# Performance work log

Hardware: AMD Instinct MI355X
Metric: run time of the kernel (lower is better)

## Reference

```python
import jax, jax.numpy as jnp
import numpy as np
from jax import lax

B, T, E = 2, 2048, 2048
H, D = 16, 128
C = H * D          # qk_dim == v_dim == 2048
K = 4              # short conv kernel size
EPS = 1e-5


def setup_inputs() -> dict:
    key = jax.random.key(0)
    ks = jax.random.split(key, 11)
    s = 0.02
    return {
        "x": jax.random.normal(ks[0], (B, T, E), dtype=jnp.float32),
        "recurrent_state": jnp.zeros((B, H, D, D), dtype=jnp.float32),
        "Wq": jax.random.normal(ks[1], (C, E), dtype=jnp.float32) * s,
        "Wk": jax.random.normal(ks[2], (C, E), dtype=jnp.float32) * s,
        "Wv": jax.random.normal(ks[3], (C, E), dtype=jnp.float32) * s,
        "Wbeta": jax.random.normal(ks[4], (H, E), dtype=jnp.float32) * s,
        "Wgate": jax.random.normal(ks[5], (C, E), dtype=jnp.float32) * s,
        "Wo": jax.random.normal(ks[6], (E, C), dtype=jnp.float32) * s,
        "wq_conv": jax.random.normal(ks[7], (C, 1, K), dtype=jnp.float32) * 0.5,
        "wk_conv": jax.random.normal(ks[8], (C, 1, K), dtype=jnp.float32) * 0.5,
        "wv_conv": jax.random.normal(ks[9], (C, 1, K), dtype=jnp.float32) * 0.5,
    }


def _causal_dwconv(u, w):
    # u: (B, T, C), w: (C, 1, K). Torch pads both sides by K-1 then truncates
    # to length T -> equivalent to causal left-pad of K-1.
    u = u.transpose(0, 2, 1)  # (B, C, T)
    y = lax.conv_general_dilated(
        u, w, window_strides=(1,), padding=[(K - 1, 0)],
        feature_group_count=C, dimension_numbers=("NCH", "OIH", "NCH"))
    return y.transpose(0, 2, 1)  # (B, T, C)


def _delta_scan(q, k, v, beta, state):
    # q,k,v: (B,T,H,D); beta: (B,T,H); state: (B,H,D,D)
    def step(S, inp):
        qt, kt, vt, bt = inp  # (B,H,D),(B,H,D),(B,H,D),(B,H)
        b = bt[..., None, None]
        S = (1.0 - b) * S + b * (kt[..., :, None] * vt[..., None, :])  # bhde
        o = jnp.einsum("bhde,bhd->bhe", S, qt)
        return S, o

    xs = (q.transpose(1, 0, 2, 3), k.transpose(1, 0, 2, 3),
          v.transpose(1, 0, 2, 3), beta.transpose(1, 0, 2))
    final_state, outs = lax.scan(step, state, xs)
    return outs.transpose(1, 0, 2, 3), final_state  # (B,T,H,D)


def reference(x, recurrent_state, Wq, Wk, Wv, Wbeta, Wgate, Wo,
              wq_conv, wk_conv, wv_conv):
    q = jax.nn.silu(_causal_dwconv(x @ Wq.T, wq_conv))
    k = jax.nn.silu(_causal_dwconv(x @ Wk.T, wk_conv))
    v = jax.nn.silu(_causal_dwconv(x @ Wv.T, wv_conv))
    beta = jax.nn.sigmoid(x @ Wbeta.T)   # (B,T,H)
    gate = jax.nn.sigmoid(x @ Wgate.T)   # (B,T,C)

    q = q.reshape(B, T, H, D) * (D ** -0.5)
    k = k.reshape(B, T, H, D)
    v = v.reshape(B, T, H, D)

    out, new_state = _delta_scan(q, k, v, beta, recurrent_state)  # (B,T,H,D)

    # GroupNorm(num_groups=H, channels=C, affine=False) over (B, C, T):
    # normalizes each (batch, head) group over its (D, T) elements.
    mean = out.mean(axis=(1, 3), keepdims=True)
    var = out.var(axis=(1, 3), keepdims=True)
    out = (out - mean) * lax.rsqrt(var + EPS)

    out = out.reshape(B, T, C) * gate
    y = out @ Wo.T  # (B,T,E)
    return y, new_state
```

## Files before the change

kernel.cpp:

```cpp
#include <hip/hip_runtime.h>
#include <hip/hip_bf16.h>
#include <math.h>

#define BB 2
#define TT 2048
#define EE 2048
#define HH 16
#define DD 128
#define CC 2048
#define KCONV 4
#define CHUNK 128
#define NC 16
#define GN_EPS 1e-5f

typedef __bf16 bf16x8 __attribute__((ext_vector_type(8)));
typedef __bf16 bf16x4 __attribute__((ext_vector_type(4)));
typedef float  f32x4  __attribute__((ext_vector_type(4)));

#define GLD16(gp, lp)                                                          \
  __builtin_amdgcn_global_load_lds(                                            \
      (const __attribute__((address_space(1))) void*)(gp),                     \
      (__attribute__((address_space(3))) void*)(lp), 16, 0, 0)

__device__ __forceinline__ bf16x8 ldfrag(const __bf16* buf, int row, int kg)
{
  return *(const bf16x8*)(buf + row * 128 + ((kg ^ (row & 7)) << 3));
}

__global__ __launch_bounds__(256)
void convert_all(const float* __restrict__ x,  const float* __restrict__ Wq,
                 const float* __restrict__ Wk, const float* __restrict__ Wv,
                 const float* __restrict__ Wg, const float* __restrict__ Wo,
                 __bf16* __restrict__ xbf, __bf16* __restrict__ Wcat,
                 __bf16* __restrict__ Wob)
{
  const int i = (blockIdx.x * 256 + threadIdx.x) * 4;
  const int XN = 8388608, WN = 4194304;
  const float* src;
  __bf16* dst;
  int off;
  if (i < XN) { src = x; dst = xbf; off = i; }
  else if (i < XN + 4 * WN) {
    const int j = i - XN;
    const int seg = j >> 22;
    src = seg == 0 ? Wq : seg == 1 ? Wk : seg == 2 ? Wv : Wg;
    dst = Wcat + ((size_t)seg << 22);
    off = j & (WN - 1);
  } else { src = Wo; dst = Wob; off = i - XN - 4 * WN; }
  const float4 v = *(const float4*)(src + off);
  bf16x4 o;
  o[0] = (__bf16)v.x; o[1] = (__bf16)v.y; o[2] = (__bf16)v.z; o[3] = (__bf16)v.w;
  *(bf16x4*)(dst + off) = o;
}

__global__ __launch_bounds__(256)
void beta_ker(const float* __restrict__ x, const float* __restrict__ Wb,
              float* __restrict__ betab)
{
  __shared__ float wsb[16 * 1024];
  const int tid = threadIdx.x;
  const int w = tid >> 6, lane = tid & 63;
  const int row = blockIdx.x * 4 + w;
  const float* xrow = x + (size_t)row * EE;

  float acc[16] = {};
#pragma unroll
  for (int kt = 0; kt < 2; ++kt) {
    __syncthreads();
#pragma unroll
    for (int it = 0; it < 16; ++it) {
      const int i = tid + it * 256;
      const int h = i >> 8, kq = i & 255;
      *(float4*)&wsb[h * 1024 + kq * 4] =
          *(const float4*)(Wb + (size_t)h * EE + kt * 1024 + kq * 4);
    }
    __syncthreads();
#pragma unroll
    for (int j = 0; j < 4; ++j) {
      const int kof = lane * 4 + j * 256;
      const float4 xv = *(const float4*)(xrow + kt * 1024 + kof);
#pragma unroll
      for (int h = 0; h < 16; ++h) {
        const float4 wv = *(const float4*)&wsb[h * 1024 + kof];
        acc[h] += xv.x * wv.x + xv.y * wv.y + xv.z * wv.z + xv.w * wv.w;
      }
    }
  }
#pragma unroll
  for (int h = 0; h < 16; ++h) {
#pragma unroll
    for (int off = 32; off; off >>= 1)
      acc[h] += __shfl_xor(acc[h], off, 64);
  }
#pragma unroll
  for (int h = 0; h < 16; ++h)
    if (lane == h)
      betab[(size_t)row * HH + h] = 1.f / (1.f + expf(-acc[h]));
}

__global__ __launch_bounds__(512)
void gemm_big(const __bf16* __restrict__ A, const __bf16* __restrict__ Bm,
              __bf16* __restrict__ o0, __bf16* __restrict__ o1,
              __bf16* __restrict__ o2, __bf16* __restrict__ o3)
{
  __shared__ __attribute__((aligned(16))) unsigned char smem[163840];
  __bf16 (*ldsA)[256 * 64] = (__bf16(*)[256 * 64])smem;
  __bf16 (*ldsB)[256 * 64] = (__bf16(*)[256 * 64])(smem + 98304);

  const int tid = threadIdx.x;
  const int w = tid >> 6, l = tid & 63;
  const int wm = w >> 2, wn = w & 3;
  const int m0 = blockIdx.y * 256, n0 = blockIdx.x * 256;
  const int NT = EE / 64;

  const int sr0 = w * 8 + (l >> 3);
  const int skg = l & 7;
  const int fr = l & 15;
  const int fkg = l >> 4;

#define STAGE_A(tile, half) do {                                               \
    const int b_ = (tile) % 3;                                                 \
    const int r0_ = sr0;                                                       \
    const int r1_ = 64 + sr0;                                                  \
    GLD16(A + (size_t)(m0 + (half) * 128 + r0_) * 2048 + (tile) * 64           \
              + ((skg ^ (r0_ & 7)) << 3),                                      \
          ldsA[b_] + ((half) * 128 + w * 8) * 64);                             \
    GLD16(A + (size_t)(m0 + (half) * 128 + r1_) * 2048 + (tile) * 64           \
              + ((skg ^ (r1_ & 7)) << 3),                                      \
          ldsA[b_] + ((half) * 128 + 64 + w * 8) * 64);                        \
  } while (0)

#define STAGE_B(tile, half) do {                                               \
    const int b_ = (tile) & 1;                                                 \
    const int r0_ = sr0;                                                       \
    const int r1_ = 64 + sr0;                                                  \
    GLD16(Bm + (size_t)(n0 + (half) * 128 + r0_) * 2048 + (tile) * 64          \
              + ((skg ^ (r0_ & 7)) << 3),                                      \
          ldsB[b_] + ((half) * 128 + w * 8) * 64);                             \
    GLD16(Bm + (size_t)(n0 + (half) * 128 + r1_) * 2048 + (tile) * 64          \
              + ((skg ^ (r1_ & 7)) << 3),                                      \
          ldsB[b_] + ((half) * 128 + 64 + w * 8) * 64);                        \
  } while (0)

#define LDA_FRAG(dst, ab, q, mf, ks) do {                                      \
    const int row_ = wm * 128 + (q) * 32 + (mf) * 16 + fr;                     \
    const int kg_ = (ks) * 4 + fkg;                                            \
    dst = *(const bf16x8*)&ldsA[ab][row_ * 64 + ((kg_ ^ (row_ & 7)) << 3)];    \
  } while (0)
#define LDB_FRAG(dst, bb, nf, ks) do {                                         \
    const int row_ = wn * 64 + (nf) * 16 + fr;                                 \
    const int kg_ = (ks) * 4 + fkg;                                            \
    dst = *(const bf16x8*)&ldsB[bb][row_ * 64 + ((kg_ ^ (row_ & 7)) << 3)];    \
  } while (0)

  f32x4 acc[8][4] = {};

  STAGE_A(0, 0); STAGE_A(0, 1); STAGE_B(0, 0); STAGE_B(0, 1);
  STAGE_A(1, 0); STAGE_A(1, 1); STAGE_B(1, 0); STAGE_B(1, 1);
  asm volatile("s_waitcnt vmcnt(8)" ::: "memory");
  __syncthreads();

  int abuf = 0;
  for (int t = 0; t < NT; ++t) {
    const int bbuf = t & 1;
    bf16x8 bfr[4][2];

    {
#pragma unroll
      for (int nf = 0; nf < 4; ++nf)
#pragma unroll
        for (int ks = 0; ks < 2; ++ks) LDB_FRAG(bfr[nf][ks], bbuf, nf, ks);
      bf16x8 af[2][2];
#pragma unroll
      for (int mf = 0; mf < 2; ++mf)
#pragma unroll
        for (int ks = 0; ks < 2; ++ks) LDA_FRAG(af[mf][ks], abuf, 0, mf, ks);
      if (t + 2 < NT) STAGE_A(t + 2, 0);
      __builtin_amdgcn_s_barrier();
      __builtin_amdgcn_s_setprio(1);
#pragma unroll
      for (int mf = 0; mf < 2; ++mf)
#pragma unroll
        for (int nf = 0; nf < 4; ++nf)
#pragma unroll
          for (int ks = 0; ks < 2; ++ks)
            acc[mf][nf] = __builtin_amdgcn_mfma_f32_16x16x32_bf16(
                af[mf][ks], bfr[nf][ks], acc[mf][nf], 0, 0, 0);
      __builtin_amdgcn_s_setprio(0);
      __builtin_amdgcn_s_barrier();
    }

#pragma unroll
    for (int q = 1; q < 4; ++q) {
      bf16x8 af[2][2];
#pragma unroll
      for (int mf = 0; mf < 2; ++mf)
#pragma unroll
        for (int ks = 0; ks < 2; ++ks) LDA_FRAG(af[mf][ks], abuf, q, mf, ks);
      if (q == 1) {
        if (t + 2 < NT) STAGE_A(t + 2, 1);
      } else if (q == 2) {
        if (t + 2 < NT) STAGE_B(t + 2, 0);
      } else {
        if (t + 2 < NT) STAGE_B(t + 2, 1);
        if (t == NT - 2) asm volatile("s_waitcnt vmcnt(0)" ::: "memory");
        else             asm volatile("s_waitcnt vmcnt(8)" ::: "memory");
      }
      __builtin_amdgcn_s_barrier();
      __builtin_amdgcn_s_setprio(1);
#pragma unroll
      for (int mf = 0; mf < 2; ++mf)
#pragma unroll
        for (int nf = 0; nf < 4; ++nf)
#pragma unroll
          for (int ks = 0; ks < 2; ++ks)
            acc[2 * q + mf][nf] = __builtin_amdgcn_mfma_f32_16x16x32_bf16(
                af[mf][ks], bfr[nf][ks], acc[2 * q + mf][nf], 0, 0, 0);
      __builtin_amdgcn_s_setprio(0);
      __builtin_amdgcn_s_barrier();
    }
    abuf = (abuf + 1 == 3) ? 0 : abuf + 1;
  }

  __syncthreads();
  const int proj = n0 >> 11;
  const int nb = n0 & 2047;
  __bf16* outp = proj == 0 ? o0 : proj == 1 ? o1 : proj == 2 ? o2 : o3;
  __bf16* ep = (__bf16*)smem + (size_t)w * 9216;
  const int crow = (l >> 4) * 4;
#pragma unroll
  for (int mf2 = 0; mf2 < 8; ++mf2)
#pragma unroll
    for (int nf = 0; nf < 4; ++nf)
#pragma unroll
      for (int r = 0; r < 4; ++r) {
        const int row = mf2 * 16 + crow + r;
        float vv = acc[mf2][nf][r];
        if (proj == 3) vv = 1.f / (1.f + expf(-vv));
        ep[row * 72 + nf * 16 + fr] = (__bf16)vv;
      }
#pragma unroll
  for (int it = 0; it < 16; ++it) {
    const int row = it * 8 + (l >> 3);
    const int c8 = (l & 7) * 8;
    const bf16x8 v8 = *(const bf16x8*)&ep[row * 72 + c8];
    *(bf16x8*)(outp + (size_t)(m0 + wm * 128 + row) * 2048 + nb + wn * 64 + c8) = v8;
  }
#undef STAGE_A
#undef STAGE_B
#undef LDA_FRAG
#undef LDB_FRAG
}

template <int ACT, typename OT>
__global__ __launch_bounds__(256)
void gemm_bf16(const __bf16* __restrict__ A, const __bf16* __restrict__ Bm,
               OT* __restrict__ Cm, int M, int N, int K)
{
  __shared__ __attribute__((aligned(16))) __bf16 As[128 * 32];
  __shared__ __attribute__((aligned(16))) __bf16 Bs[128 * 32];

  const int tid  = threadIdx.x;
  const int w    = tid >> 6;
  const int lane = tid & 63;
  const int m0 = blockIdx.y * 128, n0 = blockIdx.x * 128;
  const int wm = w >> 1, wn = w & 1;

  const int srow = lane >> 2;
  const int sk   = (lane & 3) * 8;
  const __bf16* aA0 = A  + (size_t)(m0 + w * 32 + srow) * K + sk;
  const __bf16* aA1 = aA0 + (size_t)16 * K;
  const __bf16* aB0 = Bm + (size_t)(n0 + w * 32 + srow) * K + sk;
  const __bf16* aB1 = aB0 + (size_t)16 * K;
  __bf16* lA0 = As + (w * 2 + 0) * 512;
  __bf16* lA1 = As + (w * 2 + 1) * 512;
  __bf16* lB0 = Bs + (w * 2 + 0) * 512;
  __bf16* lB1 = Bs + (w * 2 + 1) * 512;

  const int fr = lane & 15;
  const int fk = (lane >> 4) * 8;
  const __bf16* rA = As + (size_t)(wm * 64 + fr) * 32 + fk;
  const __bf16* rB = Bs + (size_t)(wn * 64 + fr) * 32 + fk;

  f32x4 acc[4][4] = {};

  for (int k0 = 0; k0 < K; k0 += 32) {
    __syncthreads();
    GLD16(aA0, lA0); GLD16(aA1, lA1);
    GLD16(aB0, lB0); GLD16(aB1, lB1);
    aA0 += 32; aA1 += 32; aB0 += 32; aB1 += 32;
    asm volatile("s_waitcnt vmcnt(0)" ::: "memory");
    __syncthreads();

    bf16x8 af[4], bfr[4];
#pragma unroll
    for (int i = 0; i < 4; ++i) af[i]  = *(const bf16x8*)(rA + i * 512);
#pragma unroll
    for (int j = 0; j < 4; ++j) bfr[j] = *(const bf16x8*)(rB + j * 512);
#pragma unroll
    for (int i = 0; i < 4; ++i)
#pragma unroll
      for (int j = 0; j < 4; ++j)
        acc[i][j] = __builtin_amdgcn_mfma_f32_16x16x32_bf16(af[i], bfr[j], acc[i][j], 0, 0, 0);
  }

  const int crow0 = (lane >> 4) * 4;
#pragma unroll
  for (int i = 0; i < 4; ++i) {
#pragma unroll
    for (int j = 0; j < 4; ++j) {
      const int n = n0 + wn * 64 + j * 16 + fr;
#pragma unroll
      for (int r = 0; r < 4; ++r) {
        const int m = m0 + wm * 64 + i * 16 + crow0 + r;
        float vv = acc[i][j][r];
        if (ACT == 1) vv = 1.f / (1.f + expf(-vv));
        Cm[(size_t)m * N + n] = (OT)vv;
      }
    }
  }
}

__global__ __launch_bounds__(256)
void conv_all(const __bf16* __restrict__ u0, const __bf16* __restrict__ u1,
              const __bf16* __restrict__ u2, const float* __restrict__ w0,
              const float* __restrict__ w1, const float* __restrict__ w2,
              __bf16* __restrict__ d0, __bf16* __restrict__ d1,
              __bf16* __restrict__ d2, float qscale)
{
  const int which = blockIdx.y;
  const __bf16* u = which == 0 ? u0 : which == 1 ? u1 : u2;
  const float* wconv = which == 0 ? w0 : which == 1 ? w1 : w2;
  __bf16* out = which == 0 ? d0 : which == 1 ? d1 : d2;
  const float scale = which == 0 ? qscale : 1.f;

  const int idx = blockIdx.x * 256 + threadIdx.x;
  const int c8 = (idx & (CC / 8 - 1)) * 8;
  const int t  = (idx >> 8) & (TT - 1);
  const int b  = idx >> 19;
  const size_t base = ((size_t)(b * TT + t)) * CC + c8;

  const bf16x8 z = {};
  const bf16x8 uu0 = *(const bf16x8*)(u + base);
  const bf16x8 uu1 = (t >= 1) ? *(const bf16x8*)(u + base - CC)     : z;
  const bf16x8 uu2 = (t >= 2) ? *(const bf16x8*)(u + base - 2 * CC) : z;
  const bf16x8 uu3 = (t >= 3) ? *(const bf16x8*)(u + base - 3 * CC) : z;

  bf16x8 o;
#pragma unroll
  for (int jj = 0; jj < 8; ++jj) {
    const float4 wv = *(const float4*)(wconv + (size_t)(c8 + jj) * 4);
    const float vv = wv.x * (float)uu3[jj] + wv.y * (float)uu2[jj]
                   + wv.z * (float)uu1[jj] + wv.w * (float)uu0[jj];
    o[jj] = (__bf16)(vv / (1.f + expf(-vv)) * scale);
  }
  *(bf16x8*)(out + base) = o;
}

__global__ __launch_bounds__(256)
void tr_kv(const __bf16* __restrict__ ksrc, const __bf16* __restrict__ vsrc,
           __bf16* __restrict__ kdst, __bf16* __restrict__ vdst)
{
  const int t0 = blockIdx.x * 64, d0 = blockIdx.y * 64;
  const int zz = blockIdx.z;
  const int bh = zz & 31, b = bh >> 4, h = bh & 15;
  const __bf16* src = (zz >= 32) ? vsrc : ksrc;
  __bf16* dst = (zz >= 32) ? vdst : kdst;
  const int tid = threadIdx.x;
  __shared__ __attribute__((aligned(16))) __bf16 tile[64][72];

#pragma unroll
  for (int it = 0; it < 2; ++it) {
    const int idx = tid + it * 256;
    const int tl = idx >> 3, g = idx & 7;
    const bf16x8 v = *(const bf16x8*)(src + ((size_t)(b * TT + t0 + tl)) * CC + h * DD + d0 + g * 8);
    *(bf16x8*)&tile[tl][g * 8] = v;
  }
  __syncthreads();
#pragma unroll
  for (int it = 0; it < 2; ++it) {
    const int idx = tid + it * 256;
    const int dl = idx >> 3, g = idx & 7;
    bf16x8 o;
#pragma unroll
    for (int jj = 0; jj < 8; ++jj) o[jj] = tile[g * 8 + jj][dl];
    *(bf16x8*)(dst + ((size_t)(bh * DD + d0 + dl)) * TT + t0 + g * 8) = o;
  }
}

__global__ __launch_bounds__(256)
void tr_f32(const float* __restrict__ in, float* __restrict__ out)
{
  const int r0 = blockIdx.x * 64, c0 = blockIdx.y * 64;
  const int bh = blockIdx.z;
  const int tid = threadIdx.x;
  __shared__ float tile[64][65];

#pragma unroll
  for (int it = 0; it < 4; ++it) {
    const int idx = tid + it * 256;
    const int rl = idx >> 4, g = idx & 15;
    const float4 v = *(const float4*)(in + (size_t)bh * 16384 + (r0 + rl) * 128 + c0 + g * 4);
    tile[rl][g * 4 + 0] = v.x; tile[rl][g * 4 + 1] = v.y;
    tile[rl][g * 4 + 2] = v.z; tile[rl][g * 4 + 3] = v.w;
  }
  __syncthreads();
#pragma unroll
  for (int it = 0; it < 4; ++it) {
    const int idx = tid + it * 256;
    const int cl = idx >> 4, g = idx & 15;
    float4 o;
    o.x = tile[g * 4 + 0][cl]; o.y = tile[g * 4 + 1][cl];
    o.z = tile[g * 4 + 2][cl]; o.w = tile[g * 4 + 3][cl];
    *(float4*)(out + (size_t)bh * 16384 + (c0 + cl) * 128 + r0 + g * 4) = o;
  }
}

__global__ __launch_bounds__(256)
void phaseA_mfma(const __bf16* __restrict__ kT, const __bf16* __restrict__ vT,
                 const float* __restrict__ beta, float* __restrict__ contribT,
                 float* __restrict__ decay)
{
  const int c = blockIdx.x, h = blockIdx.y, b = blockIdx.z;
  const int bh = b * HH + h;
  const int tid = threadIdx.x;
  const int w = tid >> 6, lane = tid & 63;
  const int wm = w >> 1, wn = w & 1;

  __shared__ __attribute__((aligned(16))) __bf16 bufVT[128 * 128];
  __shared__ __attribute__((aligned(16))) __bf16 bufKW[128 * 128];
  __shared__ float lc[CHUNK], bsh[CHUNK], wgt[CHUNK];

  {
    const __bf16* vbase = vT + ((size_t)bh * DD) * TT + c * CHUNK;
#pragma unroll
    for (int jj = 0; jj < 8; ++jj) {
      const int row = w * 32 + jj * 4 + (lane >> 4);
      const int g = lane & 15;
      GLD16(vbase + (size_t)row * TT + ((g ^ (row & 7)) << 3),
            bufVT + (w * 32 + jj * 4) * 128);
    }
  }

  if (tid < CHUNK) {
    const float bv = beta[(size_t)(b * TT + c * CHUNK + tid) * HH + h];
    bsh[tid] = bv;
    lc[tid] = log1pf(-bv);
  }
  __syncthreads();
  for (int off = 1; off < CHUNK; off <<= 1) {
    float add = 0.f;
    if (tid < CHUNK && tid >= off) add = lc[tid - off];
    __syncthreads();
    if (tid < CHUNK) lc[tid] += add;
    __syncthreads();
  }
  const float lend = lc[CHUNK - 1];
  if (tid < CHUNK) wgt[tid] = bsh[tid] * expf(lend - lc[tid]);
  if (tid == 0) decay[(size_t)bh * NC + c] = expf(lend);
  __syncthreads();

  {
    const __bf16* kbase = kT + ((size_t)bh * DD) * TT + c * CHUNK;
#pragma unroll
    for (int it = 0; it < 8; ++it) {
      const int idx = tid + it * 256;
      const int d = idx >> 4, g = idx & 15;
      const bf16x8 kv = *(const bf16x8*)(kbase + (size_t)d * TT + g * 8);
      bf16x8 o;
#pragma unroll
      for (int jj = 0; jj < 8; ++jj)
        o[jj] = (__bf16)((float)kv[jj] * wgt[g * 8 + jj]);
      *(bf16x8*)(bufKW + d * 128 + ((g ^ (d & 7)) << 3)) = o;
    }
  }
  asm volatile("s_waitcnt vmcnt(0)" ::: "memory");
  __syncthreads();

  f32x4 acc[4][4] = {};
#pragma unroll
  for (int ks = 0; ks < 4; ++ks) {
    bf16x8 a[4], bq[4];
    const int kg = ks * 4 + (lane >> 4);
#pragma unroll
    for (int f = 0; f < 4; ++f) a[f]  = ldfrag(bufVT, wm * 64 + f * 16 + (lane & 15), kg);
#pragma unroll
    for (int f = 0; f < 4; ++f) bq[f] = ldfrag(bufKW, wn * 64 + f * 16 + (lane & 15), kg);
#pragma unroll
    for (int i = 0; i < 4; ++i)
#pragma unroll
      for (int j = 0; j < 4; ++j)
        acc[i][j] = __builtin_amdgcn_mfma_f32_16x16x32_bf16(a[i], bq[j], acc[i][j], 0, 0, 0);
  }

  float* cp = contribT + ((size_t)(bh * NC + c) << 14);
  const int crow = (lane >> 4) * 4;
#pragma unroll
  for (int i = 0; i < 4; ++i)
#pragma unroll
    for (int j = 0; j < 4; ++j) {
      const int dd = wn * 64 + j * 16 + (lane & 15);
#pragma unroll
      for (int r = 0; r < 4; ++r) {
        const int e = wm * 64 + i * 16 + crow + r;
        cp[(size_t)e * 128 + dd] = acc[i][j][r];
      }
    }
}

__global__ __launch_bounds__(256)
void phaseB_T(const float* __restrict__ state0T, const float* __restrict__ contribT,
              const float* __restrict__ decay, __bf16* __restrict__ statesT,
              float* __restrict__ stateOutT)
{
  const size_t gid = (size_t)blockIdx.x * 256 + threadIdx.x;
  const int bh = (int)(gid >> 14);
  float s = state0T[gid];
  const float* dc = decay + (size_t)bh * NC;
  const int ed = (int)(gid & 16383);
#pragma unroll
  for (int c = 0; c < NC; ++c) {
    const size_t off = ((size_t)(bh * NC + c) << 14) + ed;
    statesT[off] = (__bf16)s;
    s = fmaf(dc[c], s, contribT[off]);
  }
  stateOutT[gid] = s;
}

__global__ __launch_bounds__(256)
void phaseC_mfma(const __bf16* __restrict__ qb, const __bf16* __restrict__ kb,
                 const __bf16* __restrict__ vT, const float* __restrict__ beta,
                 const __bf16* __restrict__ statesT, float* __restrict__ att,
                 float* __restrict__ partials)
{
  const int c = blockIdx.x, h = blockIdx.y, b = blockIdx.z;
  const int bh = b * HH + h;
  const int tid = threadIdx.x;
  const int w = tid >> 6, lane = tid & 63;
  const int wm = w >> 1, wn = w & 1;

  __shared__ __attribute__((aligned(16))) __bf16 bufQ[128 * 128];
  __shared__ __attribute__((aligned(16))) __bf16 bufB[128 * 128];
  __shared__ float lc[CHUNK], bsh[CHUNK];
  __shared__ float s1[256], s2[256];

  {
    const __bf16* qbase = qb + ((size_t)(b * TT + c * CHUNK)) * CC + h * DD;
    const __bf16* kbase = kb + ((size_t)(b * TT + c * CHUNK)) * CC + h * DD;
#pragma unroll
    for (int jj = 0; jj < 8; ++jj) {
      const int row = w * 32 + jj * 4 + (lane >> 4);
      const int g = lane & 15;
      GLD16(qbase + (size_t)row * CC + ((g ^ (row & 7)) << 3),
            bufQ + (w * 32 + jj * 4) * 128);
      GLD16(kbase + (size_t)row * CC + ((g ^ (row & 7)) << 3),
            bufB + (w * 32 + jj * 4) * 128);
    }
  }

  if (tid < CHUNK) {
    const float bv = beta[(size_t)(b * TT + c * CHUNK + tid) * HH + h];
    bsh[tid] = bv;
    lc[tid] = log1pf(-bv);
  }
  __syncthreads();
  for (int off = 1; off < CHUNK; off <<= 1) {
    float add = 0.f;
    if (tid < CHUNK && tid >= off) add = lc[tid - off];
    __syncthreads();
    if (tid < CHUNK) lc[tid] += add;
    __syncthreads();
  }

  asm volatile("s_waitcnt vmcnt(0)" ::: "memory");
  __syncthreads();

  f32x4 accS[4][4] = {};
#pragma unroll
  for (int ks = 0; ks < 4; ++ks) {
    bf16x8 a[4], bq[4];
    const int kg = ks * 4 + (lane >> 4);
#pragma unroll
    for (int f = 0; f < 4; ++f) a[f]  = ldfrag(bufQ, wm * 64 + f * 16 + (lane & 15), kg);
#pragma unroll
    for (int f = 0; f < 4; ++f) bq[f] = ldfrag(bufB, wn * 64 + f * 16 + (lane & 15), kg);
#pragma unroll
    for (int i = 0; i < 4; ++i)
#pragma unroll
      for (int j = 0; j < 4; ++j)
        accS[i][j] = __builtin_amdgcn_mfma_f32_16x16x32_bf16(a[i], bq[j], accS[i][j], 0, 0, 0);
  }

  __syncthreads();
  {
    const __bf16* sbase = statesT + ((size_t)(bh * NC + c) << 14);
#pragma unroll
    for (int jj = 0; jj < 8; ++jj) {
      const int row = w * 32 + jj * 4 + (lane >> 4);
      const int g = lane & 15;
      GLD16(sbase + (size_t)row * 128 + ((g ^ (row & 7)) << 3),
            bufB + (w * 32 + jj * 4) * 128);
    }
  }
  asm volatile("s_waitcnt vmcnt(0)" ::: "memory");
  __syncthreads();

  f32x4 accO[4][4] = {};
#pragma unroll
  for (int ks = 0; ks < 4; ++ks) {
    bf16x8 a[4], bq[4];
    const int kg = ks * 4 + (lane >> 4);
#pragma unroll
    for (int f = 0; f < 4; ++f) a[f]  = ldfrag(bufQ, wm * 64 + f * 16 + (lane & 15), kg);
#pragma unroll
    for (int f = 0; f < 4; ++f) bq[f] = ldfrag(bufB, wn * 64 + f * 16 + (lane & 15), kg);
#pragma unroll
    for (int i = 0; i < 4; ++i)
#pragma unroll
      for (int j = 0; j < 4; ++j)
        accO[i][j] = __builtin_amdgcn_mfma_f32_16x16x32_bf16(a[i], bq[j], accO[i][j], 0, 0, 0);
  }
  const int crow = (lane >> 4) * 4;
#pragma unroll
  for (int i = 0; i < 4; ++i)
#pragma unroll
    for (int r = 0; r < 4; ++r) {
      const float el = expf(lc[wm * 64 + i * 16 + crow + r]);
#pragma unroll
      for (int j = 0; j < 4; ++j) accO[i][j][r] *= el;
    }

  __syncthreads();
  {
    const __bf16* vbase = vT + ((size_t)bh * DD) * TT + c * CHUNK;
#pragma unroll
    for (int jj = 0; jj < 8; ++jj) {
      const int row = w * 32 + jj * 4 + (lane >> 4);
      const int g = lane & 15;
      GLD16(vbase + (size_t)row * TT + ((g ^ (row & 7)) << 3),
            bufB + (w * 32 + jj * 4) * 128);
    }
  }
  {
    float lcs[4], bss[4];
#pragma unroll
    for (int j = 0; j < 4; ++j) {
      const int s = wn * 64 + j * 16 + (lane & 15);
      lcs[j] = lc[s]; bss[j] = bsh[s];
    }
#pragma unroll
    for (int i = 0; i < 4; ++i)
#pragma unroll
      for (int r = 0; r < 4; ++r) {
        const int t = wm * 64 + i * 16 + crow + r;
        const float lct = lc[t];
#pragma unroll
        for (int j = 0; j < 4; ++j) {
          const int s = wn * 64 + j * 16 + (lane & 15);
          float p = 0.f;
          if (s <= t) p = accS[i][j][r] * bss[j] * expf(lct - lcs[j]);
          bufQ[t * 128 + (((s >> 3) ^ (t & 7)) << 3) + (s & 7)] = (__bf16)p;
        }
      }
  }
  asm volatile("s_waitcnt vmcnt(0)" ::: "memory");
  __syncthreads();

#pragma unroll
  for (int ks = 0; ks < 4; ++ks) {
    bf16x8 a[4], bq[4];
    const int kg = ks * 4 + (lane >> 4);
#pragma unroll
    for (int f = 0; f < 4; ++f) a[f]  = ldfrag(bufQ, wm * 64 + f * 16 + (lane & 15), kg);
#pragma unroll
    for (int f = 0; f < 4; ++f) bq[f] = ldfrag(bufB, wn * 64 + f * 16 + (lane & 15), kg);
#pragma unroll
    for (int i = 0; i < 4; ++i)
#pragma unroll
      for (int j = 0; j < 4; ++j)
        accO[i][j] = __builtin_amdgcn_mfma_f32_16x16x32_bf16(a[i], bq[j], accO[i][j], 0, 0, 0);
  }

  float lsum = 0.f, lsq = 0.f;
  float* obase = att + ((size_t)(b * TT + c * CHUNK)) * CC + h * DD;
#pragma unroll
  for (int i = 0; i < 4; ++i)
#pragma unroll
    for (int j = 0; j < 4; ++j) {
      const int e = wn * 64 + j * 16 + (lane & 15);
#pragma unroll
      for (int r = 0; r < 4; ++r) {
        const int t = wm * 64 + i * 16 + crow + r;
        const float vv = accO[i][j][r];
        obase[(size_t)t * CC + e] = vv;
        lsum += vv;
        lsq  += vv * vv;
      }
    }
  s1[tid] = lsum; s2[tid] = lsq;
  __syncthreads();
  for (int off = 128; off; off >>= 1) {
    if (tid < off) { s1[tid] += s1[tid + off]; s2[tid] += s2[tid + off]; }
    __syncthreads();
  }
  if (tid == 0) {
    partials[(size_t)(bh * NC + c) * 2]     = s1[0];
    partials[(size_t)(bh * NC + c) * 2 + 1] = s2[0];
  }
}

__global__ __launch_bounds__(64)
void gn_combine(const float* __restrict__ partials, float* __restrict__ stats)
{
  const int bh = blockIdx.x;
  const int lane = threadIdx.x;
  float s = 0.f, q = 0.f;
  if (lane < NC) {
    s = partials[(size_t)(bh * NC + lane) * 2];
    q = partials[(size_t)(bh * NC + lane) * 2 + 1];
  }
#pragma unroll
  for (int off = 8; off; off >>= 1) {
    s += __shfl_xor(s, off, 64);
    q += __shfl_xor(q, off, 64);
  }
  if (lane == 0) {
    const float n = (float)(TT * DD);
    const float mean = s / n;
    const float var = q / n - mean * mean;
    stats[bh * 2] = mean;
    stats[bh * 2 + 1] = rsqrtf(var + GN_EPS);
  }
}

__global__ __launch_bounds__(256)
void norm_gate(const float* __restrict__ att, const __bf16* __restrict__ gate,
               const float* __restrict__ stats, __bf16* __restrict__ g)
{
  const size_t gid = ((size_t)blockIdx.x * 256 + threadIdx.x) * 4;
  if (gid >= (size_t)BB * TT * CC) return;
  const int cpos = (int)(gid % CC);
  const int b = (int)(gid / ((size_t)TT * CC));
  const int bh = b * HH + (cpos >> 7);
  const float mean = stats[bh * 2], rstd = stats[bh * 2 + 1];
  const float4 a = *(const float4*)(att + gid);
  const bf16x4 gt = *(const bf16x4*)(gate + gid);
  bf16x4 o;
  o[0] = (__bf16)((a.x - mean) * rstd * (float)gt[0]);
  o[1] = (__bf16)((a.y - mean) * rstd * (float)gt[1]);
  o[2] = (__bf16)((a.z - mean) * rstd * (float)gt[2]);
  o[3] = (__bf16)((a.w - mean) * rstd * (float)gt[3]);
  *(bf16x4*)(g + gid) = o;
}

extern "C" void kernel_launch(void* const* d_in, const int* in_sizes, int n_in,
                              void* d_out, int out_size, void* d_ws, size_t ws_size,
                              hipStream_t stream)
{
  const float* x      = (const float*)d_in[0];
  const float* st0    = (const float*)d_in[1];
  const float* Wq     = (const float*)d_in[2];
  const float* Wk     = (const float*)d_in[3];
  const float* Wv     = (const float*)d_in[4];
  const float* Wbeta  = (const float*)d_in[5];
  const float* Wgate  = (const float*)d_in[6];
  const float* Wo     = (const float*)d_in[7];
  const float* wqc    = (const float*)d_in[8];
  const float* wkc    = (const float*)d_in[9];
  const float* wvc    = (const float*)d_in[10];

  float* ws = (float*)d_ws;
  __bf16* qbf  = (__bf16*)(ws + 0);
  __bf16* kbf  = (__bf16*)(ws + 4194304);
  __bf16* vbf  = (__bf16*)(ws + 8388608);
  __bf16* u_v  = (__bf16*)(ws + 12582912);
  __bf16* kT   = (__bf16*)(ws + 12582912);
  __bf16* gbf  = (__bf16*)(ws + 12582912);
  __bf16* vT   = (__bf16*)(ws + 16777216);
  __bf16* xbf  = (__bf16*)(ws + 20971520);
  float* contribT = ws + 20971520;
  __bf16* Wcat = (__bf16*)(ws + 25165824);
  __bf16* gatebuf = (__bf16*)(ws + 33554432);
  __bf16* statesT = (__bf16*)(ws + 8388608);
  float* betab    = ws + 37748736;
  float* decay    = ws + 37814272;
  float* stats    = ws + 37814784;
  float* partials = ws + 37814848;
  float* state0T  = ws + 37815872;
  float* stateOutT= ws + 38340160;
  __bf16* Wob  = (__bf16*)(ws + 38864448);

  float* y_out  = (float*)d_out;
  float* st_out = (float*)d_out + (size_t)BB * TT * EE;
  __bf16* u_q = (__bf16*)d_out;
  __bf16* u_k = (__bf16*)d_out + 8388608;
  float* att = y_out;

  const dim3 blk(256);
  const dim3 gBig(8192 / 256, (BB * TT) / 256);
  const dim3 gB(CC / 128, (BB * TT) / 128);
  const dim3 gKV(TT / 64, DD / 64, 2 * BB * HH);
  const dim3 gTrS(2, 2, BB * HH);
  const dim3 gScan(NC, HH, BB);
  const float qscale = 0.08838834764831845f;

  convert_all<<<dim3(28672), blk, 0, stream>>>(x, Wq, Wk, Wv, Wgate, Wo,
                                               xbf, Wcat, Wob);

  beta_ker<<<dim3((BB * TT) / 4), blk, 0, stream>>>(x, Wbeta, betab);

  gemm_big<<<gBig, dim3(512), 0, stream>>>(xbf, Wcat, u_q, u_k, u_v, gatebuf);

  conv_all<<<dim3(4096, 3), blk, 0, stream>>>(u_q, u_k, u_v, wqc, wkc, wvc,
                                              qbf, kbf, vbf, qscale);

  tr_kv<<<gKV, blk, 0, stream>>>(kbf, vbf, kT, vT);

  tr_f32<<<gTrS, blk, 0, stream>>>(st0, state0T);

  phaseA_mfma<<<gScan, blk, 0, stream>>>(kT, vT, betab, contribT, decay);
  phaseB_T<<<dim3((BB * HH * DD * DD) / 256), blk, 0, stream>>>(state0T, contribT, decay, statesT, stateOutT);
  tr_f32<<<gTrS, blk, 0, stream>>>(stateOutT, st_out);
  phaseC_mfma<<<gScan, blk, 0, stream>>>(qbf, kbf, vT, betab, statesT, att, partials);

  gn_combine<<<dim3(BB * HH), dim3(64), 0, stream>>>(partials, stats);
  norm_gate<<<dim3((BB * TT * CC) / (256 * 4)), blk, 0, stream>>>(att, gatebuf, stats, gbf);

  gemm_bf16<0, float><<<gB, blk, 0, stream>>>(gbf, Wob, y_out, BB * TT, EE, CC);
}
```

Baseline: 383.5 us.

## Pipeline big GEMM loads, add tiled Wo GEMM, fuse conv with transpose

```diff
diff --git a/kernel.cpp b/kernel.cpp
--- a/kernel.cpp
+++ b/kernel.cpp
@@ -156,12 +156,12 @@
   f32x4 acc[8][4] = {};
 
   STAGE_A(0, 0); STAGE_A(0, 1); STAGE_B(0, 0); STAGE_B(0, 1);
-  STAGE_A(1, 0); STAGE_A(1, 1); STAGE_B(1, 0); STAGE_B(1, 1);
-  asm volatile("s_waitcnt vmcnt(8)" ::: "memory");
-  __syncthreads();
-
-  int abuf = 0;
+  STAGE_A(1, 0); STAGE_A(1, 1); STAGE_B(1, 0);
+  asm volatile("s_waitcnt vmcnt(6)" ::: "memory");
+  __builtin_amdgcn_s_barrier();
+
   for (int t = 0; t < NT; ++t) {
+    const int abuf = t % 3;
     const int bbuf = t & 1;
     bf16x8 bfr[4][2];
 
@@ -175,7 +175,7 @@
       for (int mf = 0; mf < 2; ++mf)
 #pragma unroll
         for (int ks = 0; ks < 2; ++ks) LDA_FRAG(af[mf][ks], abuf, 0, mf, ks);
-      if (t + 2 < NT) STAGE_A(t + 2, 0);
+      if (t + 1 < NT) STAGE_B(t + 1, 1);
       __builtin_amdgcn_s_barrier();
       __builtin_amdgcn_s_setprio(1);
 #pragma unroll
@@ -187,7 +187,6 @@
             acc[mf][nf] = __builtin_amdgcn_mfma_f32_16x16x32_bf16(
                 af[mf][ks], bfr[nf][ks], acc[mf][nf], 0, 0, 0);
       __builtin_amdgcn_s_setprio(0);
-      __builtin_amdgcn_s_barrier();
     }
 
 #pragma unroll
@@ -198,13 +197,13 @@
 #pragma unroll
         for (int ks = 0; ks < 2; ++ks) LDA_FRAG(af[mf][ks], abuf, q, mf, ks);
       if (q == 1) {
+        if (t + 2 < NT) STAGE_A(t + 2, 0);
+      } else if (q == 2) {
         if (t + 2 < NT) STAGE_A(t + 2, 1);
-      } else if (q == 2) {
+      } else {
         if (t + 2 < NT) STAGE_B(t + 2, 0);
-      } else {
-        if (t + 2 < NT) STAGE_B(t + 2, 1);
-        if (t == NT - 2) asm volatile("s_waitcnt vmcnt(0)" ::: "memory");
-        else             asm volatile("s_waitcnt vmcnt(8)" ::: "memory");
+        if (t == NT - 2)     asm volatile("s_waitcnt vmcnt(0)" ::: "memory");
+        else if (t < NT - 2) asm volatile("s_waitcnt vmcnt(6)" ::: "memory");
       }
       __builtin_amdgcn_s_barrier();
       __builtin_amdgcn_s_setprio(1);
@@ -217,9 +216,7 @@
             acc[2 * q + mf][nf] = __builtin_amdgcn_mfma_f32_16x16x32_bf16(
                 af[mf][ks], bfr[nf][ks], acc[2 * q + mf][nf], 0, 0, 0);
       __builtin_amdgcn_s_setprio(0);
-      __builtin_amdgcn_s_barrier();
-    }
-    abuf = (abuf + 1 == 3) ? 0 : abuf + 1;
+    }
   }
 
   __syncthreads();
@@ -252,120 +249,148 @@
 #undef LDB_FRAG
 }
 
-template <int ACT, typename OT>
+__global__ __launch_bounds__(512)
+void gemm_wo(const __bf16* __restrict__ A, const __bf16* __restrict__ Bm,
+             float* __restrict__ Cm)
+{
+  __shared__ __attribute__((aligned(16))) unsigned char smem[147456];
+  __bf16 (*ldsA)[128 * 64] = (__bf16(*)[128 * 64])smem;
+  __bf16 (*ldsB)[256 * 64] = (__bf16(*)[256 * 64])(smem + 49152);
+
+  const int tid = threadIdx.x;
+  const int w = tid >> 6, l = tid & 63;
+  const int wm = w >> 2, wn = w & 3;
+  const int m0 = blockIdx.y * 128, n0 = blockIdx.x * 256;
+  const int NT = CC / 64;
+
+  const int sr0 = w * 8 + (l >> 3);
+  const int skg = l & 7;
+  const int fr = l & 15;
+  const int fkg = l >> 4;
+
+#define STAGE_AW(tile) do {                                                    \
+    const int b_ = (tile) % 3;                                                 \
+    const int r0_ = sr0;                                                       \
+    const int r1_ = 64 + sr0;                                                  \
+    GLD16(A + (size_t)(m0 + r0_) * 2048 + (tile) * 64                          \
+              + ((skg ^ (r0_ & 7)) << 3),                                      \
+          ldsA[b_] + (w * 8) * 64);                                            \
+    GLD16(A + (size_t)(m0 + r1_) * 2048 + (tile) * 64                          \
+              + ((skg ^ (r1_ & 7)) << 3),                                      \
+          ldsA[b_] + (64 + w * 8) * 64);                                       \
+  } while (0)
+
+#define STAGE_BW(tile, half) do {                                              \
+    const int b_ = (tile) % 3;                                                 \
+    const int r0_ = sr0;                                                       \
+    const int r1_ = 64 + sr0;                                                  \
+    GLD16(Bm + (size_t)(n0 + (half) * 128 + r0_) * 2048 + (tile) * 64          \
+              + ((skg ^ (r0_ & 7)) << 3),                                      \
+          ldsB[b_] + ((half) * 128 + w * 8) * 64);                             \
+    GLD16(Bm + (size_t)(n0 + (half) * 128 + r1_) * 2048 + (tile) * 64          \
+              + ((skg ^ (r1_ & 7)) << 3),                                      \
+          ldsB[b_] + ((half) * 128 + 64 + w * 8) * 64);                        \
+  } while (0)
+
+#define LDA_FRAGW(dst, ab, mf, ks) do {                                        \
+    const int row_ = wm * 64 + (mf) * 16 + fr;                                 \
+    const int kg_ = (ks) * 4 + fkg;                                            \
+    dst = *(const bf16x8*)&ldsA[ab][row_ * 64 + ((kg_ ^ (row_ & 7)) << 3)];    \
+  } while (0)
+#define LDB_FRAGW(dst, bb, nf, ks) do {                                        \
+    const int row_ = wn * 64 + (nf) * 16 + fr;                                 \
+    const int kg_ = (ks) * 4 + fkg;                                            \
+    dst = *(const bf16x8*)&ldsB[bb][row_ * 64 + ((kg_ ^ (row_ & 7)) << 3)];    \
+  } while (0)
+
+  f32x4 acc[4][4] = {};
+
+  STAGE_BW(0, 0); STAGE_BW(0, 1); STAGE_AW(0);
+  STAGE_BW(1, 0); STAGE_BW(1, 1); STAGE_AW(1);
+  asm volatile("s_waitcnt vmcnt(6)" ::: "memory");
+  __builtin_amdgcn_s_barrier();
+
+  for (int t = 0; t < NT; ++t) {
+    const int buf = t % 3;
+    bf16x8 bfr[4][2];
+    bf16x8 af[2][2];
+
+#pragma unroll
+    for (int nf = 0; nf < 4; ++nf)
+#pragma unroll
+      for (int ks = 0; ks < 2; ++ks) LDB_FRAGW(bfr[nf][ks], buf, nf, ks);
+#pragma unroll
+    for (int mf = 0; mf < 2; ++mf)
+#pragma unroll
+      for (int ks = 0; ks < 2; ++ks) LDA_FRAGW(af[mf][ks], buf, mf, ks);
+    if (t + 2 < NT) { STAGE_BW(t + 2, 0); STAGE_BW(t + 2, 1); }
+    __builtin_amdgcn_s_barrier();
+    __builtin_amdgcn_s_setprio(1);
+#pragma unroll
+    for (int mf = 0; mf < 2; ++mf)
+#pragma unroll
+      for (int nf = 0; nf < 4; ++nf)
+#pragma unroll
+        for (int ks = 0; ks < 2; ++ks)
+          acc[mf][nf] = __builtin_amdgcn_mfma_f32_16x16x32_bf16(
+              af[mf][ks], bfr[nf][ks], acc[mf][nf], 0, 0, 0);
+    __builtin_amdgcn_s_setprio(0);
+
+#pragma unroll
+    for (int mf = 0; mf < 2; ++mf)
+#pragma unroll
+      for (int ks = 0; ks < 2; ++ks) LDA_FRAGW(af[mf][ks], buf, mf + 2, ks);
+    if (t + 2 < NT) STAGE_AW(t + 2);
+    if (t == NT - 2)     asm volatile("s_waitcnt vmcnt(0)" ::: "memory");
+    else if (t < NT - 2) asm volatile("s_waitcnt vmcnt(6)" ::: "memory");
+    __builtin_amdgcn_s_barrier();
+    __builtin_amdgcn_s_setprio(1);
+#pragma unroll
+    for (int mf = 0; mf < 2; ++mf)
+#pragma unroll
+      for (int nf = 0; nf < 4; ++nf)
+#pragma unroll
+        for (int ks = 0; ks < 2; ++ks)
+          acc[mf + 2][nf] = __builtin_amdgcn_mfma_f32_16x16x32_bf16(
+              af[mf][ks], bfr[nf][ks], acc[mf + 2][nf], 0, 0, 0);
+    __builtin_amdgcn_s_setprio(0);
+  }
+
+  __syncthreads();
+  float* ep = (float*)smem + (size_t)w * (64 * 68);
+  const int crow = (l >> 4) * 4;
+#pragma unroll
+  for (int mf = 0; mf < 4; ++mf)
+#pragma unroll
+    for (int nf = 0; nf < 4; ++nf)
+#pragma unroll
+      for (int r = 0; r < 4; ++r)
+        ep[(mf * 16 + crow + r) * 68 + nf * 16 + fr] = acc[mf][nf][r];
+#pragma unroll
+  for (int it = 0; it < 16; ++it) {
+    const int row = it * 4 + (l >> 4);
+    const int c4 = (l & 15) * 4;
+    const float4 v4 = *(const float4*)&ep[row * 68 + c4];
+    *(float4*)(Cm + (size_t)(m0 + wm * 64 + row) * 2048 + n0 + wn * 64 + c4) = v4;
+  }
+#undef STAGE_AW
+#undef STAGE_BW
+#undef LDA_FRAGW
+#undef LDB_FRAGW
+}
+
 __global__ __launch_bounds__(256)
-void gemm_bf16(const __bf16* __restrict__ A, const __bf16* __restrict__ Bm,
-               OT* __restrict__ Cm, int M, int N, int K)
-{
-  __shared__ __attribute__((aligned(16))) __bf16 As[128 * 32];
-  __shared__ __attribute__((aligned(16))) __bf16 Bs[128 * 32];
-
-  const int tid  = threadIdx.x;
-  const int w    = tid >> 6;
-  const int lane = tid & 63;
-  const int m0 = blockIdx.y * 128, n0 = blockIdx.x * 128;
-  const int wm = w >> 1, wn = w & 1;
-
-  const int srow = lane >> 2;
-  const int sk   = (lane & 3) * 8;
-  const __bf16* aA0 = A  + (size_t)(m0 + w * 32 + srow) * K + sk;
-  const __bf16* aA1 = aA0 + (size_t)16 * K;
-  const __bf16* aB0 = Bm + (size_t)(n0 + w * 32 + srow) * K + sk;
-  const __bf16* aB1 = aB0 + (size_t)16 * K;
-  __bf16* lA0 = As + (w * 2 + 0) * 512;
-  __bf16* lA1 = As + (w * 2 + 1) * 512;
-  __bf16* lB0 = Bs + (w * 2 + 0) * 512;
-  __bf16* lB1 = Bs + (w * 2 + 1) * 512;
-
-  const int fr = lane & 15;
-  const int fk = (lane >> 4) * 8;
-  const __bf16* rA = As + (size_t)(wm * 64 + fr) * 32 + fk;
-  const __bf16* rB = Bs + (size_t)(wn * 64 + fr) * 32 + fk;
-
-  f32x4 acc[4][4] = {};
-
-  for (int k0 = 0; k0 < K; k0 += 32) {
-    __syncthreads();
-    GLD16(aA0, lA0); GLD16(aA1, lA1);
-    GLD16(aB0, lB0); GLD16(aB1, lB1);
-    aA0 += 32; aA1 += 32; aB0 += 32; aB1 += 32;
-    asm volatile("s_waitcnt vmcnt(0)" ::: "memory");
-    __syncthreads();
-
-    bf16x8 af[4], bfr[4];
-#pragma unroll
-    for (int i = 0; i < 4; ++i) af[i]  = *(const bf16x8*)(rA + i * 512);
-#pragma unroll
-    for (int j = 0; j < 4; ++j) bfr[j] = *(const bf16x8*)(rB + j * 512);
-#pragma unroll
-    for (int i = 0; i < 4; ++i)
-#pragma unroll
-      for (int j = 0; j < 4; ++j)
-        acc[i][j] = __builtin_amdgcn_mfma_f32_16x16x32_bf16(af[i], bfr[j], acc[i][j], 0, 0, 0);
-  }
-
-  const int crow0 = (lane >> 4) * 4;
-#pragma unroll
-  for (int i = 0; i < 4; ++i) {
-#pragma unroll
-    for (int j = 0; j < 4; ++j) {
-      const int n = n0 + wn * 64 + j * 16 + fr;
-#pragma unroll
-      for (int r = 0; r < 4; ++r) {
-        const int m = m0 + wm * 64 + i * 16 + crow0 + r;
-        float vv = acc[i][j][r];
-        if (ACT == 1) vv = 1.f / (1.f + expf(-vv));
-        Cm[(size_t)m * N + n] = (OT)vv;
-      }
-    }
-  }
-}
-
-__global__ __launch_bounds__(256)
-void conv_all(const __bf16* __restrict__ u0, const __bf16* __restrict__ u1,
-              const __bf16* __restrict__ u2, const float* __restrict__ w0,
-              const float* __restrict__ w1, const float* __restrict__ w2,
-              __bf16* __restrict__ d0, __bf16* __restrict__ d1,
-              __bf16* __restrict__ d2, float qscale)
-{
-  const int which = blockIdx.y;
-  const __bf16* u = which == 0 ? u0 : which == 1 ? u1 : u2;
-  const float* wconv = which == 0 ? w0 : which == 1 ? w1 : w2;
-  __bf16* out = which == 0 ? d0 : which == 1 ? d1 : d2;
+void conv_tr(const __bf16* __restrict__ u_q, const __bf16* __restrict__ u_k,
+             const __bf16* __restrict__ u_v, const float* __restrict__ wq,
+             const float* __restrict__ wk, const float* __restrict__ wv,
+             __bf16* __restrict__ qbf, __bf16* __restrict__ kbf,
+             __bf16* __restrict__ kT, __bf16* __restrict__ vT, float qscale)
+{
+  const int t0 = blockIdx.x * 64, c0 = blockIdx.y * 64;
+  const int which = blockIdx.z / BB, b = blockIdx.z % BB;
+  const __bf16* u = which == 0 ? u_q : which == 1 ? u_k : u_v;
+  const float* wc = which == 0 ? wq : which == 1 ? wk : wv;
   const float scale = which == 0 ? qscale : 1.f;
-
-  const int idx = blockIdx.x * 256 + threadIdx.x;
-  const int c8 = (idx & (CC / 8 - 1)) * 8;
-  const int t  = (idx >> 8) & (TT - 1);
-  const int b  = idx >> 19;
-  const size_t base = ((size_t)(b * TT + t)) * CC + c8;
-
-  const bf16x8 z = {};
-  const bf16x8 uu0 = *(const bf16x8*)(u + base);
-  const bf16x8 uu1 = (t >= 1) ? *(const bf16x8*)(u + base - CC)     : z;
-  const bf16x8 uu2 = (t >= 2) ? *(const bf16x8*)(u + base - 2 * CC) : z;
-  const bf16x8 uu3 = (t >= 3) ? *(const bf16x8*)(u + base - 3 * CC) : z;
-
-  bf16x8 o;
-#pragma unroll
-  for (int jj = 0; jj < 8; ++jj) {
-    const float4 wv = *(const float4*)(wconv + (size_t)(c8 + jj) * 4);
-    const float vv = wv.x * (float)uu3[jj] + wv.y * (float)uu2[jj]
-                   + wv.z * (float)uu1[jj] + wv.w * (float)uu0[jj];
-    o[jj] = (__bf16)(vv / (1.f + expf(-vv)) * scale);
-  }
-  *(bf16x8*)(out + base) = o;
-}
-
-__global__ __launch_bounds__(256)
-void tr_kv(const __bf16* __restrict__ ksrc, const __bf16* __restrict__ vsrc,
-           __bf16* __restrict__ kdst, __bf16* __restrict__ vdst)
-{
-  const int t0 = blockIdx.x * 64, d0 = blockIdx.y * 64;
-  const int zz = blockIdx.z;
-  const int bh = zz & 31, b = bh >> 4, h = bh & 15;
-  const __bf16* src = (zz >= 32) ? vsrc : ksrc;
-  __bf16* dst = (zz >= 32) ? vdst : kdst;
   const int tid = threadIdx.x;
   __shared__ __attribute__((aligned(16))) __bf16 tile[64][72];
 
@@ -373,18 +398,40 @@
   for (int it = 0; it < 2; ++it) {
     const int idx = tid + it * 256;
     const int tl = idx >> 3, g = idx & 7;
-    const bf16x8 v = *(const bf16x8*)(src + ((size_t)(b * TT + t0 + tl)) * CC + h * DD + d0 + g * 8);
-    *(bf16x8*)&tile[tl][g * 8] = v;
-  }
-  __syncthreads();
-#pragma unroll
-  for (int it = 0; it < 2; ++it) {
-    const int idx = tid + it * 256;
-    const int dl = idx >> 3, g = idx & 7;
+    const int t = t0 + tl;
+    const int c8 = c0 + g * 8;
+    const size_t base = ((size_t)(b * TT + t)) * CC + c8;
+    const bf16x8 z = {};
+    const bf16x8 uu0 = *(const bf16x8*)(u + base);
+    const bf16x8 uu1 = (t >= 1) ? *(const bf16x8*)(u + base - CC)     : z;
+    const bf16x8 uu2 = (t >= 2) ? *(const bf16x8*)(u + base - 2 * CC) : z;
+    const bf16x8 uu3 = (t >= 3) ? *(const bf16x8*)(u + base - 3 * CC) : z;
     bf16x8 o;
 #pragma unroll
-    for (int jj = 0; jj < 8; ++jj) o[jj] = tile[g * 8 + jj][dl];
-    *(bf16x8*)(dst + ((size_t)(bh * DD + d0 + dl)) * TT + t0 + g * 8) = o;
+    for (int jj = 0; jj < 8; ++jj) {
+      const float4 wv4 = *(const float4*)(wc + (size_t)(c8 + jj) * 4);
+      const float vv = wv4.x * (float)uu3[jj] + wv4.y * (float)uu2[jj]
+                     + wv4.z * (float)uu1[jj] + wv4.w * (float)uu0[jj];
+      o[jj] = (__bf16)(vv / (1.f + expf(-vv)) * scale);
+    }
+    if (which == 0) *(bf16x8*)(qbf + base) = o;
+    if (which == 1) *(bf16x8*)(kbf + base) = o;
+    if (which >= 1) *(bf16x8*)&tile[tl][g * 8] = o;
+  }
+  if (which >= 1) {
+    __syncthreads();
+    const int h = c0 >> 7, d0 = c0 & 127;
+    const int bh = b * HH + h;
+    __bf16* dst = (which == 1) ? kT : vT;
+#pragma unroll
+    for (int it = 0; it < 2; ++it) {
+      const int idx = tid + it * 256;
+      const int dl = idx >> 3, g = idx & 7;
+      bf16x8 o;
+#pragma unroll
+      for (int jj = 0; jj < 8; ++jj) o[jj] = tile[g * 8 + jj][dl];
+      *(bf16x8*)(dst + ((size_t)(bh * DD + d0 + dl)) * TT + t0 + g * 8) = o;
+    }
   }
 }
 
@@ -772,8 +819,8 @@
   float* ws = (float*)d_ws;
   __bf16* qbf  = (__bf16*)(ws + 0);
   __bf16* kbf  = (__bf16*)(ws + 4194304);
-  __bf16* vbf  = (__bf16*)(ws + 8388608);
-  __bf16* u_v  = (__bf16*)(ws + 12582912);
+  __bf16* u_v  = (__bf16*)(ws + 8388608);
+  __bf16* statesT = (__bf16*)(ws + 8388608);
   __bf16* kT   = (__bf16*)(ws + 12582912);
   __bf16* gbf  = (__bf16*)(ws + 12582912);
   __bf16* vT   = (__bf16*)(ws + 16777216);
@@ -781,7 +828,6 @@
   float* contribT = ws + 20971520;
   __bf16* Wcat = (__bf16*)(ws + 25165824);
   __bf16* gatebuf = (__bf16*)(ws + 33554432);
-  __bf16* statesT = (__bf16*)(ws + 8388608);
   float* betab    = ws + 37748736;
   float* decay    = ws + 37814272;
   float* stats    = ws + 37814784;
@@ -798,8 +844,8 @@
 
   const dim3 blk(256);
   const dim3 gBig(8192 / 256, (BB * TT) / 256);
-  const dim3 gB(CC / 128, (BB * TT) / 128);
-  const dim3 gKV(TT / 64, DD / 64, 2 * BB * HH);
+  const dim3 gWo(EE / 256, (BB * TT) / 128);
+  const dim3 gConv(TT / 64, CC / 64, 3 * BB);
   const dim3 gTrS(2, 2, BB * HH);
   const dim3 gScan(NC, HH, BB);
   const float qscale = 0.08838834764831845f;
@@ -811,10 +857,8 @@
 
   gemm_big<<<gBig, dim3(512), 0, stream>>>(xbf, Wcat, u_q, u_k, u_v, gatebuf);
 
-  conv_all<<<dim3(4096, 3), blk, 0, stream>>>(u_q, u_k, u_v, wqc, wkc, wvc,
-                                              qbf, kbf, vbf, qscale);
-
-  tr_kv<<<gKV, blk, 0, stream>>>(kbf, vbf, kT, vT);
+  conv_tr<<<gConv, blk, 0, stream>>>(u_q, u_k, u_v, wqc, wkc, wvc,
+                                     qbf, kbf, kT, vT, qscale);
 
   tr_f32<<<gTrS, blk, 0, stream>>>(st0, state0T);
 
@@ -826,5 +870,5 @@
   gn_combine<<<dim3(BB * HH), dim3(64), 0, stream>>>(partials, stats);
   norm_gate<<<dim3((BB * TT * CC) / (256 * 4)), blk, 0, stream>>>(att, gatebuf, stats, gbf);
 
-  gemm_bf16<0, float><<<gB, blk, 0, stream>>>(gbf, Wob, y_out, BB * TT, EE, CC);
-}
+  gemm_wo<<<gWo, dim3(512), 0, stream>>>(gbf, Wob, y_out);
+}
```

After: 332.9 us. 1.15x faster.
